# Kernel tuning notes

Measured on AMD Instinct MI355X. Metric: run time of the kernel, lower is better.

Reference implementation:

```python
import jax, jax.numpy as jnp
import numpy as np

N_HEADS = 16
SCALE = 0.25  # hard-coded in the torch module


def setup_inputs() -> dict:
    key = jax.random.key(0)
    ks = jax.random.split(key, 5)
    B, S, D = 2, 2048, 1024
    std = 1.0 / np.sqrt(D)
    return {
        "x": jax.random.normal(ks[0], (B, S, D), dtype=jnp.float32),
        "wq": jax.random.normal(ks[1], (D, D), dtype=jnp.float32) * std,
        "wk": jax.random.normal(ks[2], (D, D), dtype=jnp.float32) * std,
        "wv": jax.random.normal(ks[3], (D, D), dtype=jnp.float32) * std,
        "wo": jax.random.normal(ks[4], (D, D), dtype=jnp.float32) * std,
    }


def reference(x, wq, wk, wv, wo):
    B, S, D = x.shape
    H = N_HEADS
    hd = D // H
    # torch Linear(no bias): y = x @ W.T ; weights stored [out, in]
    q = (x @ wq.T).reshape(B, S, H, hd).transpose(0, 2, 1, 3)  # [B,H,S,hd]
    k = (x @ wk.T).reshape(B, S, H, hd).transpose(0, 2, 1, 3)
    v = (x @ wv.T).reshape(B, S, H, hd).transpose(0, 2, 1, 3)

    scores = jnp.einsum("bhqd,bhkd->bhqk", q, k) * SCALE  # [B,H,S,S]
    idx = jnp.arange(S)
    q_idx = idx[:, None]
    kv_idx = idx[None, :]
    # ALiBi-style score_mod: score - |q_idx - kv_idx|
    bias = -jnp.abs(q_idx - kv_idx).astype(scores.dtype)  # [S,S]
    causal = q_idx >= kv_idx  # [S,S]
    scores = jnp.where(causal, scores + bias, -jnp.inf)
    attn = jax.nn.softmax(scores, axis=-1)
    out = jnp.einsum("bhqk,bhkd->bhqd", attn, v)  # [B,H,S,hd]
    out = out.transpose(0, 2, 1, 3).reshape(B, S, D)
    return out @ wo.T
```

## Files before the change

### kernel.cpp

```cpp
#include <hip/hip_runtime.h>
#include <hip/hip_bf16.h>
#include <stdint.h>

typedef __bf16 bf16x8 __attribute__((ext_vector_type(8)));
typedef __bf16 bf16x4 __attribute__((ext_vector_type(4)));
typedef float  f32x4  __attribute__((ext_vector_type(4)));
typedef uint32_t u32x4 __attribute__((ext_vector_type(4)));

#define LOG2E 1.44269504088896f

__device__ __forceinline__ void glds16(const __bf16* g, __bf16* l) {
  __builtin_amdgcn_global_load_lds((const __attribute__((address_space(1))) void*)g,
                                   (__attribute__((address_space(3))) void*)l, 16, 0, 0);
}

__device__ __forceinline__ uint32_t pk2(float lo, float hi) {
  __bf16 l = (__bf16)lo, h = (__bf16)hi;
  uint16_t lb = __builtin_bit_cast(uint16_t, l);
  uint16_t hb = __builtin_bit_cast(uint16_t, h);
  return ((uint32_t)hb << 16) | lb;
}

__global__ __launch_bounds__(256) void cvt_all(
    const float* __restrict__ x,  const float* __restrict__ wq,
    const float* __restrict__ wk, const float* __restrict__ wv,
    const float* __restrict__ wo,
    __bf16* __restrict__ xb,  __bf16* __restrict__ wqb,
    __bf16* __restrict__ wkb, __bf16* __restrict__ wvb,
    __bf16* __restrict__ wob) {
  int i = blockIdx.x * 256 + threadIdx.x;
  const float* src; __bf16* dst; int j;
  if (i < 1048576) { src = x; dst = xb; j = i; }
  else {
    int t = i - 1048576;
    int w = t >> 18;
    j = t & 262143;
    src = (w == 0) ? wq : (w == 1) ? wk : (w == 2) ? wv : wo;
    dst = (w == 0) ? wqb : (w == 1) ? wkb : (w == 2) ? wvb : wob;
  }
  float4 v = ((const float4*)src)[j];
  bf16x4 o = { (__bf16)v.x, (__bf16)v.y, (__bf16)v.z, (__bf16)v.w };
  ((bf16x4*)dst)[j] = o;
}


__global__ __launch_bounds__(256, 2)
void qkv_gemm(const __bf16* __restrict__ A,
              const __bf16* __restrict__ Wq, const __bf16* __restrict__ Wk,
              const __bf16* __restrict__ Wv,
              __bf16* __restrict__ Qo, __bf16* __restrict__ Ko,
              __bf16* __restrict__ Vo) {
  __shared__ __bf16 As[3][128 * 32];
  __shared__ __bf16 Bs[3][192 * 32];
  const int tid  = threadIdx.x;
  const int lane = tid & 63;
  const int wv   = tid >> 6;
  const int l15  = lane & 15, lg = lane >> 4;
  const int wr   = (wv >> 1) << 6;
  const int wc   = (wv & 1) * 96;
  const long rowBase = (long)blockIdx.y * 128;
  const int  colBase = blockIdx.x * 192;

  const __bf16* aSrc[2]; int aOffL[2];
#pragma unroll
  for (int i = 0; i < 2; ++i) {
    int c = i * 256 + tid;
    int row = c >> 2;
    int lc = ((c & 3) - (row >> 1)) & 3;
    aSrc[i] = A + (rowBase + row) * 1024 + lc * 8;
    aOffL[i] = c * 8;
  }
  const __bf16* bSrc[3]; int bOffL[3];
#pragma unroll
  for (int i = 0; i < 3; ++i) {
    int c = i * 256 + tid;
    int row = c >> 2;
    int lc = ((c & 3) - (row >> 1)) & 3;
    int g = colBase + row;
    const __bf16* Wsel = (g < 1024) ? (Wq + (long)g * 1024)
                       : (g < 2048) ? (Wk + (long)(g - 1024) * 1024)
                                    : (Wv + (long)(g - 2048) * 1024);
    bSrc[i] = Wsel + lc * 8;
    bOffL[i] = c * 8;
  }
  int aOff[4], bOff[6];
#pragma unroll
  for (int t = 0; t < 4; ++t) {
    int rA = wr + t * 16 + l15;
    aOff[t] = rA * 32 + (((lg + (rA >> 1)) & 3) << 3);
  }
#pragma unroll
  for (int n = 0; n < 6; ++n) {
    int rB = wc + n * 16 + l15;
    bOff[n] = rB * 32 + (((lg + (rB >> 1)) & 3) << 3);
  }

  f32x4 acc[4][6] = {};
#pragma unroll
  for (int i = 0; i < 2; ++i) glds16(aSrc[i], &As[0][aOffL[i]]);
#pragma unroll
  for (int i = 0; i < 3; ++i) glds16(bSrc[i], &Bs[0][bOffL[i]]);
#pragma unroll
  for (int i = 0; i < 2; ++i) glds16(aSrc[i] + 32, &As[1][aOffL[i]]);
#pragma unroll
  for (int i = 0; i < 3; ++i) glds16(bSrc[i] + 32, &Bs[1][bOffL[i]]);
  asm volatile("s_waitcnt vmcnt(5)" ::: "memory");
  __builtin_amdgcn_s_barrier();
  __builtin_amdgcn_sched_barrier(0);

  int cur = 0;
  for (int kt = 0; kt < 32; ++kt) {
    bf16x8 af[4], bfr[6];
#pragma unroll
    for (int t = 0; t < 4; ++t) af[t] = *(const bf16x8*)(&As[cur][aOff[t]]);
#pragma unroll
    for (int n = 0; n < 6; ++n) bfr[n] = *(const bf16x8*)(&Bs[cur][bOff[n]]);
    if (kt < 30) {
      int nb = cur + 2; if (nb >= 3) nb -= 3;
      const int k2 = (kt + 2) << 5;
#pragma unroll
      for (int i = 0; i < 2; ++i) glds16(aSrc[i] + k2, &As[nb][aOffL[i]]);
#pragma unroll
      for (int i = 0; i < 3; ++i) glds16(bSrc[i] + k2, &Bs[nb][bOffL[i]]);
    }
    __builtin_amdgcn_s_setprio(1);
#pragma unroll
    for (int mi = 0; mi < 4; ++mi)
#pragma unroll
      for (int ni = 0; ni < 6; ++ni)
        acc[mi][ni] = __builtin_amdgcn_mfma_f32_16x16x32_bf16(af[mi], bfr[ni], acc[mi][ni], 0, 0, 0);
    __builtin_amdgcn_s_setprio(0);
    if (kt < 31) {
      if (kt < 30) asm volatile("s_waitcnt vmcnt(5)" ::: "memory");
      else         asm volatile("s_waitcnt vmcnt(0)" ::: "memory");
      __builtin_amdgcn_s_barrier();
      __builtin_amdgcn_sched_barrier(0);
    }
    cur += 1; if (cur >= 3) cur -= 3;
  }

#pragma unroll
  for (int mi = 0; mi < 4; ++mi)
#pragma unroll
    for (int ni = 0; ni < 6; ++ni) {
      int colg = colBase + wc + ni * 16;
      int whichc = colg >> 10;
      if (whichc == 2) {
        long row = rowBase + wr + mi * 16 + (lg << 2);
        long col = (colg - 2048) + l15;
        long idx = ((row >> 11) * 1024 + col) * 2048 + (row & 2047);
        bf16x4 o = { (__bf16)acc[mi][ni][0], (__bf16)acc[mi][ni][1],
                     (__bf16)acc[mi][ni][2], (__bf16)acc[mi][ni][3] };
        *(bf16x4*)(&Vo[idx]) = o;
      } else {
        __bf16* dstp = (whichc == 0) ? Qo : Ko;
        long col = (colg & 1023) + l15;
#pragma unroll
        for (int r = 0; r < 4; ++r) {
          long row = rowBase + wr + mi * 16 + (lg << 2) + r;
          dstp[row * 1024 + col] = (__bf16)acc[mi][ni][r];
        }
      }
    }
}

__global__ __launch_bounds__(256, 2)
void wo_gemm(const __bf16* __restrict__ A, const __bf16* __restrict__ W,
             float* __restrict__ C) {
  __shared__ __bf16 As[3][64 * 32];
  __shared__ __bf16 Bs[3][128 * 32];
  const int tid  = threadIdx.x;
  const int lane = tid & 63;
  const int wv   = tid >> 6;
  const int l15  = lane & 15, lg = lane >> 4;
  const int wc   = wv << 5;
  const long rowBase = (long)blockIdx.y * 64;
  const long colBase = (long)blockIdx.x * 128;

  int arow = tid >> 2;
  int alc = ((tid & 3) - (arow >> 1)) & 3;
  const __bf16* aSrc = A + (rowBase + arow) * 1024 + alc * 8;
  int aOffL = tid * 8;
  const __bf16* bSrc[2]; int bOffL[2];
#pragma unroll
  for (int i = 0; i < 2; ++i) {
    int c = i * 256 + tid;
    int row = c >> 2;
    int lc = ((c & 3) - (row >> 1)) & 3;
    bSrc[i] = W + (colBase + row) * 1024 + lc * 8;
    bOffL[i] = c * 8;
  }
  int aOff[4], bOff[2];
#pragma unroll
  for (int t = 0; t < 4; ++t) {
    int rA = t * 16 + l15;
    aOff[t] = rA * 32 + (((lg + (rA >> 1)) & 3) << 3);
  }
#pragma unroll
  for (int n = 0; n < 2; ++n) {
    int rB = wc + n * 16 + l15;
    bOff[n] = rB * 32 + (((lg + (rB >> 1)) & 3) << 3);
  }

  f32x4 acc[4][2] = {};
  glds16(aSrc, &As[0][aOffL]);
#pragma unroll
  for (int i = 0; i < 2; ++i) glds16(bSrc[i], &Bs[0][bOffL[i]]);
  glds16(aSrc + 32, &As[1][aOffL]);
#pragma unroll
  for (int i = 0; i < 2; ++i) glds16(bSrc[i] + 32, &Bs[1][bOffL[i]]);
  asm volatile("s_waitcnt vmcnt(3)" ::: "memory");
  __builtin_amdgcn_s_barrier();
  __builtin_amdgcn_sched_barrier(0);

  int cur = 0;
  for (int kt = 0; kt < 32; ++kt) {
    bf16x8 af[4], bfr[2];
#pragma unroll
    for (int t = 0; t < 4; ++t) af[t] = *(const bf16x8*)(&As[cur][aOff[t]]);
#pragma unroll
    for (int n = 0; n < 2; ++n) bfr[n] = *(const bf16x8*)(&Bs[cur][bOff[n]]);
    if (kt < 30) {
      int nb = cur + 2; if (nb >= 3) nb -= 3;
      const int k2 = (kt + 2) << 5;
      glds16(aSrc + k2, &As[nb][aOffL]);
#pragma unroll
      for (int i = 0; i < 2; ++i) glds16(bSrc[i] + k2, &Bs[nb][bOffL[i]]);
    }
    __builtin_amdgcn_s_setprio(1);
#pragma unroll
    for (int mi = 0; mi < 4; ++mi)
#pragma unroll
      for (int ni = 0; ni < 2; ++ni)
        acc[mi][ni] = __builtin_amdgcn_mfma_f32_16x16x32_bf16(af[mi], bfr[ni], acc[mi][ni], 0, 0, 0);
    __builtin_amdgcn_s_setprio(0);
    if (kt < 31) {
      if (kt < 30) asm volatile("s_waitcnt vmcnt(3)" ::: "memory");
      else         asm volatile("s_waitcnt vmcnt(0)" ::: "memory");
      __builtin_amdgcn_s_barrier();
      __builtin_amdgcn_sched_barrier(0);
    }
    cur += 1; if (cur >= 3) cur -= 3;
  }

#pragma unroll
  for (int mi = 0; mi < 4; ++mi)
#pragma unroll
    for (int ni = 0; ni < 2; ++ni)
#pragma unroll
      for (int r = 0; r < 4; ++r) {
        long row = rowBase + mi * 16 + (lg << 2) + r;
        long col = colBase + wc + ni * 16 + l15;
        C[row * 1024 + col] = acc[mi][ni][r];
      }
}

#define LOADK(kv, dst)                                                         \
  dst[0] = *(const bf16x8*)(Kb + (long)((kv) + l15) * D + lg * 8);             \
  dst[1] = *(const bf16x8*)(Kb + (long)((kv) + l15) * D + 32 + lg * 8);        \
  dst[2] = *(const bf16x8*)(Kb + (long)((kv) + 16 + l15) * D + lg * 8);        \
  dst[3] = *(const bf16x8*)(Kb + (long)((kv) + 16 + l15) * D + 32 + lg * 8);
#define LOADV(kv, dst)                                                         \
  _Pragma("unroll")                                                            \
  for (int dg = 0; dg < 4; ++dg)                                               \
    dst[dg] = *(const bf16x8*)(Vb + (long)(dg * 16 + l15) * S + (kv) + lg * 8);

__global__ __launch_bounds__(256, 2)
void attn64(const __bf16* __restrict__ Q, const __bf16* __restrict__ Kk,
            const __bf16* __restrict__ VT, __bf16* __restrict__ O) {
  constexpr int S = 2048, D = 1024;
  constexpr float C0 = 0.25f * LOG2E;
  constexpr float FM = 14.0f;
  const int lane = threadIdx.x & 63;
  const int wv   = threadIdx.x >> 6;
  const int q0   = blockIdx.x * 128 + wv * 32;
  const int h = blockIdx.y, b = blockIdx.z;
  const __bf16* Qb = Q  + (long)b * S * D + h * 64;
  const __bf16* Kb = Kk + (long)b * S * D + h * 64;
  const __bf16* Vb = VT + (long)(b * 16 + h) * 64 * S;
  const int l15 = lane & 15, lg = lane >> 4;

  bf16x8 qf[2][2];
#pragma unroll
  for (int g = 0; g < 2; ++g) {
    qf[g][0] = *(const bf16x8*)(Qb + (long)(q0 + 16 * g + l15) * D + lg * 8);
    qf[g][1] = *(const bf16x8*)(Qb + (long)(q0 + 16 * g + l15) * D + 32 + lg * 8);
  }

  f32x4 acc[2][4] = {};
  float lsum[2] = {0.f, 0.f};

  const int srcA = l15 + ((lane & 16) ? 32 : 0);
  const int srcB = srcA + 16;
  const bool hi  = (lg >= 2);

  int kvb = (q0 > 192) ? ((q0 - 192) & ~31) : 0;
  bf16x8 ck[4], cv[4], nk[4], nv[4];
  LOADK(kvb, ck); LOADV(kvb, cv);

  for (; kvb <= q0; kvb += 32) {
    const bool more = (kvb + 32 <= q0);
    if (more) { LOADK(kvb + 32, nk); LOADV(kvb + 32, nv); }

    f32x4 sa[2], sb[2];
    __builtin_amdgcn_s_setprio(1);
#pragma unroll
    for (int g = 0; g < 2; ++g) {
      f32x4 za = {}, zb = {};
      za = __builtin_amdgcn_mfma_f32_16x16x32_bf16(ck[0], qf[g][0], za, 0, 0, 0);
      za = __builtin_amdgcn_mfma_f32_16x16x32_bf16(ck[1], qf[g][1], za, 0, 0, 0);
      zb = __builtin_amdgcn_mfma_f32_16x16x32_bf16(ck[2], qf[g][0], zb, 0, 0, 0);
      zb = __builtin_amdgcn_mfma_f32_16x16x32_bf16(ck[3], qf[g][1], zb, 0, 0, 0);
      sa[g] = za; sb[g] = zb;
    }
    __builtin_amdgcn_s_setprio(0);

    const bool diag = (kvb == q0);
#pragma unroll
    for (int g = 0; g < 2; ++g) {
      const int qg = q0 + 16 * g;
      float bL = ((float)(kvb + 4 * lg - qg - l15) - FM) * LOG2E;
      float ea[4], eb[4];
      if (!diag) {
#pragma unroll
        for (int r = 0; r < 4; ++r) {
          ea[r] = exp2f(fmaf(sa[g][r], C0, bL + (float)r * LOG2E));
          eb[r] = exp2f(fmaf(sb[g][r], C0, bL + (float)(r + 16) * LOG2E));
          lsum[g] += ea[r] + eb[r];
        }
      } else {
        int dc = l15 - 4 * lg;
#pragma unroll
        for (int r = 0; r < 4; ++r) {
          if (g == 0) {
            ea[r] = (r <= dc) ? exp2f(fmaf(sa[g][r], C0, bL + (float)r * LOG2E)) : 0.f;
            eb[r] = 0.f;
          } else {
            ea[r] = exp2f(fmaf(sa[g][r], C0, bL + (float)r * LOG2E));
            eb[r] = (r <= dc) ? exp2f(fmaf(sb[g][r], C0, bL + (float)(r + 16) * LOG2E)) : 0.f;
          }
          lsum[g] += ea[r] + eb[r];
        }
      }
      uint32_t wa0 = pk2(ea[0], ea[1]), wa1 = pk2(ea[2], ea[3]);
      uint32_t wb0 = pk2(eb[0], eb[1]), wb1 = pk2(eb[2], eb[3]);
      uint32_t a0 = __shfl(wa0, srcA), a1 = __shfl(wa1, srcA);
      uint32_t a2 = __shfl(wa0, srcB), a3 = __shfl(wa1, srcB);
      uint32_t b0 = __shfl(wb0, srcA), b1 = __shfl(wb1, srcA);
      uint32_t b2 = __shfl(wb0, srcB), b3 = __shfl(wb1, srcB);
      u32x4 wt = { hi ? b0 : a0, hi ? b1 : a1, hi ? b2 : a2, hi ? b3 : a3 };
      bf16x8 pf = __builtin_bit_cast(bf16x8, wt);

      __builtin_amdgcn_s_setprio(1);
#pragma unroll
      for (int dg = 0; dg < 4; ++dg)
        acc[g][dg] = __builtin_amdgcn_mfma_f32_16x16x32_bf16(cv[dg], pf, acc[g][dg], 0, 0, 0);
      __builtin_amdgcn_s_setprio(0);
    }

    if (more) {
#pragma unroll
      for (int i = 0; i < 4; ++i) { ck[i] = nk[i]; cv[i] = nv[i]; }
    }
  }

#pragma unroll
  for (int g = 0; g < 2; ++g) {
    float s = lsum[g];
    s += __shfl_xor(s, 16);
    s += __shfl_xor(s, 32);
    float inv = 1.0f / s;
    int row = q0 + 16 * g + l15;
#pragma unroll
    for (int dg = 0; dg < 4; ++dg) {
      bf16x4 o = { (__bf16)(acc[g][dg][0] * inv), (__bf16)(acc[g][dg][1] * inv),
                   (__bf16)(acc[g][dg][2] * inv), (__bf16)(acc[g][dg][3] * inv) };
      *(bf16x4*)(&O[((long)b * S + row) * D + h * 64 + dg * 16 + 4 * lg]) = o;
    }
  }
}

extern "C" void kernel_launch(void* const* d_in, const int* in_sizes, int n_in,
                              void* d_out, int out_size, void* d_ws, size_t ws_size,
                              hipStream_t stream) {
  const float* x  = (const float*)d_in[0];
  const float* wq = (const float*)d_in[1];
  const float* wk = (const float*)d_in[2];
  const float* wv = (const float*)d_in[3];
  const float* wo = (const float*)d_in[4];
  float* out = (float*)d_out;
  char* ws = (char*)d_ws;
  const long MB = 1 << 20;
  __bf16* xb  = (__bf16*)(ws + 0 * MB);
  __bf16* wqb = (__bf16*)(ws + 8 * MB);
  __bf16* wkb = (__bf16*)(ws + 10 * MB);
  __bf16* wvb = (__bf16*)(ws + 12 * MB);
  __bf16* wob = (__bf16*)(ws + 14 * MB);
  __bf16* Qb  = (__bf16*)(ws + 16 * MB);
  __bf16* Kb  = (__bf16*)(ws + 24 * MB);
  __bf16* VTb = (__bf16*)(ws + 32 * MB);
  __bf16* Ab  = (__bf16*)(ws + 40 * MB);

  cvt_all<<<8192, 256, 0, stream>>>(x, wq, wk, wv, wo, xb, wqb, wkb, wvb, wob);
  qkv_gemm<<<dim3(16, 32), 256, 0, stream>>>(xb, wqb, wkb, wvb, Qb, Kb, VTb);
  attn64<<<dim3(16, 16, 2), 256, 0, stream>>>(Qb, Kb, VTb, Ab);
  wo_gemm<<<dim3(8, 64), 256, 0, stream>>>(Ab, wob, out);
}
```

Baseline: 82.77 us.

## Switch projection GEMMs to BK=64 double-buffered LDS pipeline

Both the QKV and output-projection GEMMs move from a triple-buffered K-tile of 32 to a double-buffered K-tile of 64, with an 8-chunk XOR swizzle adapted to the wider rows. This halves the number of barriers and main-loop iterations and issues more MFMAs per sync, aiming to cut synchronization overhead. In exchange the prefetch distance drops to one stage with a full vmcnt(0) wait, so more load latency may be exposed. LDS use per block also rises, which may limit occupancy.

```diff
diff --git a/kernel.cpp b/kernel.cpp
--- a/kernel.cpp
+++ b/kernel.cpp
@@ -50,8 +50,8 @@
               const __bf16* __restrict__ Wv,
               __bf16* __restrict__ Qo, __bf16* __restrict__ Ko,
               __bf16* __restrict__ Vo) {
-  __shared__ __bf16 As[3][128 * 32];
-  __shared__ __bf16 Bs[3][192 * 32];
+  __shared__ __bf16 As[2][128 * 64];
+  __shared__ __bf16 Bs[2][192 * 64];
   const int tid  = threadIdx.x;
   const int lane = tid & 63;
   const int wv   = tid >> 6;
@@ -61,21 +61,21 @@
   const long rowBase = (long)blockIdx.y * 128;
   const int  colBase = blockIdx.x * 192;
 
-  const __bf16* aSrc[2]; int aOffL[2];
-#pragma unroll
-  for (int i = 0; i < 2; ++i) {
+  const __bf16* aSrc[4]; int aOffL[4];
+#pragma unroll
+  for (int i = 0; i < 4; ++i) {
     int c = i * 256 + tid;
-    int row = c >> 2;
-    int lc = ((c & 3) - (row >> 1)) & 3;
+    int row = c >> 3;
+    int lc = ((c & 7) - row) & 7;
     aSrc[i] = A + (rowBase + row) * 1024 + lc * 8;
     aOffL[i] = c * 8;
   }
-  const __bf16* bSrc[3]; int bOffL[3];
-#pragma unroll
-  for (int i = 0; i < 3; ++i) {
+  const __bf16* bSrc[6]; int bOffL[6];
+#pragma unroll
+  for (int i = 0; i < 6; ++i) {
     int c = i * 256 + tid;
-    int row = c >> 2;
-    int lc = ((c & 3) - (row >> 1)) & 3;
+    int row = c >> 3;
+    int lc = ((c & 7) - row) & 7;
     int g = colBase + row;
     const __bf16* Wsel = (g < 1024) ? (Wq + (long)g * 1024)
                        : (g < 2048) ? (Wk + (long)(g - 1024) * 1024)
@@ -83,60 +83,59 @@
     bSrc[i] = Wsel + lc * 8;
     bOffL[i] = c * 8;
   }
-  int aOff[4], bOff[6];
-#pragma unroll
-  for (int t = 0; t < 4; ++t) {
-    int rA = wr + t * 16 + l15;
-    aOff[t] = rA * 32 + (((lg + (rA >> 1)) & 3) << 3);
-  }
-#pragma unroll
-  for (int n = 0; n < 6; ++n) {
-    int rB = wc + n * 16 + l15;
-    bOff[n] = rB * 32 + (((lg + (rB >> 1)) & 3) << 3);
+  int aOff[2][4], bOff[2][6];
+#pragma unroll
+  for (int kc = 0; kc < 2; ++kc) {
+#pragma unroll
+    for (int t = 0; t < 4; ++t) {
+      int rA = wr + t * 16 + l15;
+      aOff[kc][t] = rA * 64 + (((kc * 4 + lg + rA) & 7) << 3);
+    }
+#pragma unroll
+    for (int n = 0; n < 6; ++n) {
+      int rB = wc + n * 16 + l15;
+      bOff[kc][n] = rB * 64 + (((kc * 4 + lg + rB) & 7) << 3);
+    }
   }
 
   f32x4 acc[4][6] = {};
 #pragma unroll
-  for (int i = 0; i < 2; ++i) glds16(aSrc[i], &As[0][aOffL[i]]);
-#pragma unroll
-  for (int i = 0; i < 3; ++i) glds16(bSrc[i], &Bs[0][bOffL[i]]);
-#pragma unroll
-  for (int i = 0; i < 2; ++i) glds16(aSrc[i] + 32, &As[1][aOffL[i]]);
-#pragma unroll
-  for (int i = 0; i < 3; ++i) glds16(bSrc[i] + 32, &Bs[1][bOffL[i]]);
-  asm volatile("s_waitcnt vmcnt(5)" ::: "memory");
+  for (int i = 0; i < 4; ++i) glds16(aSrc[i], &As[0][aOffL[i]]);
+#pragma unroll
+  for (int i = 0; i < 6; ++i) glds16(bSrc[i], &Bs[0][bOffL[i]]);
+  asm volatile("s_waitcnt vmcnt(0)" ::: "memory");
   __builtin_amdgcn_s_barrier();
   __builtin_amdgcn_sched_barrier(0);
 
-  int cur = 0;
-  for (int kt = 0; kt < 32; ++kt) {
-    bf16x8 af[4], bfr[6];
-#pragma unroll
-    for (int t = 0; t < 4; ++t) af[t] = *(const bf16x8*)(&As[cur][aOff[t]]);
-#pragma unroll
-    for (int n = 0; n < 6; ++n) bfr[n] = *(const bf16x8*)(&Bs[cur][bOff[n]]);
-    if (kt < 30) {
-      int nb = cur + 2; if (nb >= 3) nb -= 3;
-      const int k2 = (kt + 2) << 5;
-#pragma unroll
-      for (int i = 0; i < 2; ++i) glds16(aSrc[i] + k2, &As[nb][aOffL[i]]);
-#pragma unroll
-      for (int i = 0; i < 3; ++i) glds16(bSrc[i] + k2, &Bs[nb][bOffL[i]]);
-    }
-    __builtin_amdgcn_s_setprio(1);
-#pragma unroll
-    for (int mi = 0; mi < 4; ++mi)
-#pragma unroll
-      for (int ni = 0; ni < 6; ++ni)
-        acc[mi][ni] = __builtin_amdgcn_mfma_f32_16x16x32_bf16(af[mi], bfr[ni], acc[mi][ni], 0, 0, 0);
-    __builtin_amdgcn_s_setprio(0);
-    if (kt < 31) {
-      if (kt < 30) asm volatile("s_waitcnt vmcnt(5)" ::: "memory");
-      else         asm volatile("s_waitcnt vmcnt(0)" ::: "memory");
+  for (int kt = 0; kt < 16; ++kt) {
+    const int cur = kt & 1;
+    if (kt < 15) {
+      const int k1 = (kt + 1) << 6;
+#pragma unroll
+      for (int i = 0; i < 4; ++i) glds16(aSrc[i] + k1, &As[cur ^ 1][aOffL[i]]);
+#pragma unroll
+      for (int i = 0; i < 6; ++i) glds16(bSrc[i] + k1, &Bs[cur ^ 1][bOffL[i]]);
+    }
+#pragma unroll
+    for (int kc = 0; kc < 2; ++kc) {
+      bf16x8 af[4], bfr[6];
+#pragma unroll
+      for (int t = 0; t < 4; ++t) af[t] = *(const bf16x8*)(&As[cur][aOff[kc][t]]);
+#pragma unroll
+      for (int n = 0; n < 6; ++n) bfr[n] = *(const bf16x8*)(&Bs[cur][bOff[kc][n]]);
+      __builtin_amdgcn_s_setprio(1);
+#pragma unroll
+      for (int mi = 0; mi < 4; ++mi)
+#pragma unroll
+        for (int ni = 0; ni < 6; ++ni)
+          acc[mi][ni] = __builtin_amdgcn_mfma_f32_16x16x32_bf16(af[mi], bfr[ni], acc[mi][ni], 0, 0, 0);
+      __builtin_amdgcn_s_setprio(0);
+    }
+    if (kt < 15) {
+      asm volatile("s_waitcnt vmcnt(0)" ::: "memory");
       __builtin_amdgcn_s_barrier();
       __builtin_amdgcn_sched_barrier(0);
     }
-    cur += 1; if (cur >= 3) cur -= 3;
   }
 
 #pragma unroll
@@ -167,8 +166,8 @@
 __global__ __launch_bounds__(256, 2)
 void wo_gemm(const __bf16* __restrict__ A, const __bf16* __restrict__ W,
              float* __restrict__ C) {
-  __shared__ __bf16 As[3][64 * 32];
-  __shared__ __bf16 Bs[3][128 * 32];
+  __shared__ __bf16 As[2][64 * 64];
+  __shared__ __bf16 Bs[2][128 * 64];
   const int tid  = threadIdx.x;
   const int lane = tid & 63;
   const int wv   = tid >> 6;
@@ -177,70 +176,77 @@
   const long rowBase = (long)blockIdx.y * 64;
   const long colBase = (long)blockIdx.x * 128;
 
-  int arow = tid >> 2;
-  int alc = ((tid & 3) - (arow >> 1)) & 3;
-  const __bf16* aSrc = A + (rowBase + arow) * 1024 + alc * 8;
-  int aOffL = tid * 8;
-  const __bf16* bSrc[2]; int bOffL[2];
+  const __bf16* aSrc[2]; int aOffL[2];
 #pragma unroll
   for (int i = 0; i < 2; ++i) {
     int c = i * 256 + tid;
-    int row = c >> 2;
-    int lc = ((c & 3) - (row >> 1)) & 3;
+    int row = c >> 3;
+    int lc = ((c & 7) - row) & 7;
+    aSrc[i] = A + (rowBase + row) * 1024 + lc * 8;
+    aOffL[i] = c * 8;
+  }
+  const __bf16* bSrc[4]; int bOffL[4];
+#pragma unroll
+  for (int i = 0; i < 4; ++i) {
+    int c = i * 256 + tid;
+    int row = c >> 3;
+    int lc = ((c & 7) - row) & 7;
     bSrc[i] = W + (colBase + row) * 1024 + lc * 8;
     bOffL[i] = c * 8;
   }
-  int aOff[4], bOff[2];
-#pragma unroll
-  for (int t = 0; t < 4; ++t) {
-    int rA = t * 16 + l15;
-    aOff[t] = rA * 32 + (((lg + (rA >> 1)) & 3) << 3);
-  }
-#pragma unroll
-  for (int n = 0; n < 2; ++n) {
-    int rB = wc + n * 16 + l15;
-    bOff[n] = rB * 32 + (((lg + (rB >> 1)) & 3) << 3);
+  int aOff[2][4], bOff[2][2];
+#pragma unroll
+  for (int kc = 0; kc < 2; ++kc) {
+#pragma unroll
+    for (int t = 0; t < 4; ++t) {
+      int rA = t * 16 + l15;
+      aOff[kc][t] = rA * 64 + (((kc * 4 + lg + rA) & 7) << 3);
+    }
+#pragma unroll
+    for (int n = 0; n < 2; ++n) {
+      int rB = wc + n * 16 + l15;
+      bOff[kc][n] = rB * 64 + (((kc * 4 + lg + rB) & 7) << 3);
+    }
   }
 
   f32x4 acc[4][2] = {};
-  glds16(aSrc, &As[0][aOffL]);
-#pragma unroll
-  for (int i = 0; i < 2; ++i) glds16(bSrc[i], &Bs[0][bOffL[i]]);
-  glds16(aSrc + 32, &As[1][aOffL]);
-#pragma unroll
-  for (int i = 0; i < 2; ++i) glds16(bSrc[i] + 32, &Bs[1][bOffL[i]]);
-  asm volatile("s_waitcnt vmcnt(3)" ::: "memory");
+#pragma unroll
+  for (int i = 0; i < 2; ++i) glds16(aSrc[i], &As[0][aOffL[i]]);
+#pragma unroll
+  for (int i = 0; i < 4; ++i) glds16(bSrc[i], &Bs[0][bOffL[i]]);
+  asm volatile("s_waitcnt vmcnt(0)" ::: "memory");
   __builtin_amdgcn_s_barrier();
   __builtin_amdgcn_sched_barrier(0);
 
-  int cur = 0;
-  for (int kt = 0; kt < 32; ++kt) {
-    bf16x8 af[4], bfr[2];
-#pragma unroll
-    for (int t = 0; t < 4; ++t) af[t] = *(const bf16x8*)(&As[cur][aOff[t]]);
-#pragma unroll
-    for (int n = 0; n < 2; ++n) bfr[n] = *(const bf16x8*)(&Bs[cur][bOff[n]]);
-    if (kt < 30) {
-      int nb = cur + 2; if (nb >= 3) nb -= 3;
-      const int k2 = (kt + 2) << 5;
-      glds16(aSrc + k2, &As[nb][aOffL]);
-#pragma unroll
-      for (int i = 0; i < 2; ++i) glds16(bSrc[i] + k2, &Bs[nb][bOffL[i]]);
-    }
-    __builtin_amdgcn_s_setprio(1);
-#pragma unroll
-    for (int mi = 0; mi < 4; ++mi)
-#pragma unroll
-      for (int ni = 0; ni < 2; ++ni)
-        acc[mi][ni] = __builtin_amdgcn_mfma_f32_16x16x32_bf16(af[mi], bfr[ni], acc[mi][ni], 0, 0, 0);
-    __builtin_amdgcn_s_setprio(0);
-    if (kt < 31) {
-      if (kt < 30) asm volatile("s_waitcnt vmcnt(3)" ::: "memory");
-      else         asm volatile("s_waitcnt vmcnt(0)" ::: "memory");
+  for (int kt = 0; kt < 16; ++kt) {
+    const int cur = kt & 1;
+    if (kt < 15) {
+      const int k1 = (kt + 1) << 6;
+#pragma unroll
+      for (int i = 0; i < 2; ++i) glds16(aSrc[i] + k1, &As[cur ^ 1][aOffL[i]]);
+#pragma unroll
+      for (int i = 0; i < 4; ++i) glds16(bSrc[i] + k1, &Bs[cur ^ 1][bOffL[i]]);
+    }
+#pragma unroll
+    for (int kc = 0; kc < 2; ++kc) {
+      bf16x8 af[4], bfr[2];
+#pragma unroll
+      for (int t = 0; t < 4; ++t) af[t] = *(const bf16x8*)(&As[cur][aOff[kc][t]]);
+#pragma unroll
+      for (int n = 0; n < 2; ++n) bfr[n] = *(const bf16x8*)(&Bs[cur][bOff[kc][n]]);
+      __builtin_amdgcn_s_setprio(1);
+#pragma unroll
+      for (int mi = 0; mi < 4; ++mi)
+#pragma unroll
+        for (int ni = 0; ni < 2; ++ni)
+          acc[mi][ni] = __builtin_amdgcn_mfma_f32_16x16x32_bf16(af[mi], bfr[ni], acc[mi][ni], 0, 0, 0);
+      __builtin_amdgcn_s_setprio(0);
+    }
+    if (kt < 15) {
+      asm volatile("s_waitcnt vmcnt(0)" ::: "memory");
       __builtin_amdgcn_s_barrier();
       __builtin_amdgcn_sched_barrier(0);
     }
-    cur += 1; if (cur >= 3) cur -= 3;
   }
 
 #pragma unroll
```

Measured after the change: 80.79 us. 2.4% less time.
